# Optimization experiments

Hardware: AMD Instinct MI355X
Metric: run time of the kernel (lower is better)

The kernel has to match this reference:

```python
import jax, jax.numpy as jnp
import numpy as np


def setup_inputs() -> dict:
    key = jax.random.key(0)
    B, S, D, H = 4, 2048, 1024, 16
    hd = D // H
    ks = jax.random.split(key, 11)
    sc = 1.0 / np.sqrt(D)
    return {
        "keys": jax.random.normal(ks[0], (B, S, D), jnp.float32),
        "queries": jax.random.normal(ks[1], (B, S, D), jnp.float32),
        "values": jax.random.normal(ks[2], (B, S, D), jnp.float32),
        "Wq": jax.random.normal(ks[3], (H, D, hd), jnp.float32) * sc,
        "bq": jax.random.normal(ks[4], (H, hd), jnp.float32) * 0.02,
        "Wk": jax.random.normal(ks[5], (H, D, hd), jnp.float32) * sc,
        "bk": jax.random.normal(ks[6], (H, hd), jnp.float32) * 0.02,
        "Wv": jax.random.normal(ks[7], (H, D, hd), jnp.float32) * sc,
        "bv": jax.random.normal(ks[8], (H, hd), jnp.float32) * 0.02,
        "Wo": jax.random.normal(ks[9], (D, D), jnp.float32) * sc,
        "bo": jax.random.normal(ks[10], (D,), jnp.float32) * 0.02,
    }


def reference(keys, queries, values, Wq, bq, Wk, bk, Wv, bv, Wo, bo):
    # Per-head linear projections: [B,S,D] x [H,D,hd] -> [B,H,S,hd]
    q = jnp.einsum("bsd,hde->bhse", queries, Wq) + bq[None, :, None, :]
    k = jnp.einsum("bsd,hde->bhse", keys, Wk) + bk[None, :, None, :]
    v = jnp.einsum("bsd,hde->bhse", values, Wv) + bv[None, :, None, :]

    hd = q.shape[-1]
    S = q.shape[2]
    scores = jnp.einsum("bhse,bhte->bhst", q, k) / jnp.sqrt(jnp.float32(hd))
    causal = jnp.tril(jnp.ones((S, S), dtype=bool))  # tril buffer
    scores = jnp.where(causal[None, None, :, :], scores, -jnp.inf)
    attn = jax.nn.softmax(scores, axis=-1)  # dropout p=0 (eval)

    o = jnp.einsum("bhst,bhte->bhse", attn, v)  # [B,H,S,hd]
    # concat heads -> [B,S,H*hd]
    o = o.transpose(0, 2, 1, 3).reshape(o.shape[0], S, -1)
    return o @ Wo + bo
```

## Files before the change

### kernel.cpp

```cpp
#include <hip/hip_runtime.h>
#include <stdint.h>

typedef unsigned short u16;
typedef __attribute__((ext_vector_type(4))) float f32x4;
typedef __attribute__((ext_vector_type(8))) short bfrag;

static __device__ __forceinline__ u16 f2bf(float f) {
  union { float f; uint32_t u; } v; v.f = f;
  return (u16)((v.u + 0x7fffu + ((v.u >> 16) & 1u)) >> 16);
}
static __device__ __forceinline__ uint32_t cvtpk(float lo, float hi) {
  uint32_t r;
  asm("v_cvt_pk_bf16_f32 %0, %1, %2" : "=v"(r) : "v"(lo), "v"(hi));
  return r;
}
static __device__ __forceinline__ uint32_t pk2bf(float lo, float hi) {
  union { float f; uint32_t u; } a, b; a.f = lo; b.f = hi;
  return __builtin_amdgcn_perm(b.u + 0x8000u, a.u + 0x8000u, 0x07060302u);
}
static __device__ __forceinline__ float fexp2(float x) {
  float r;
  asm("v_exp_f32 %0, %1" : "=v"(r) : "v"(x));
  return r;
}

#define GLOAD16(gp, lp)                                              \
  __builtin_amdgcn_global_load_lds(                                  \
      (const __attribute__((address_space(1))) uint32_t*)(gp),       \
      (__attribute__((address_space(3))) uint32_t*)(lp), 16, 0, 0)

__global__ __launch_bounds__(256) void pack_w_hde(const float* __restrict__ W,
                                                  u16* __restrict__ Wt) {
  __shared__ float tile[64][65];
  const int h = blockIdx.y, k0 = blockIdx.x * 64;
  const int tid = threadIdx.x;
#pragma unroll
  for (int j = 0; j < 4; ++j) {
    int idx = tid + j * 256;
    int rr = idx >> 4, c4 = (idx & 15) * 4;
    const float4 v = *(const float4*)(W + (size_t)h * 65536 + (size_t)(k0 + rr) * 64 + c4);
    tile[rr][c4 + 0] = v.x; tile[rr][c4 + 1] = v.y;
    tile[rr][c4 + 2] = v.z; tile[rr][c4 + 3] = v.w;
  }
  __syncthreads();
#pragma unroll
  for (int j = 0; j < 4; ++j) {
    int idx = tid + j * 256;
    int ee = idx >> 4, c4 = (idx & 15) * 4;
    uint2 u;
    u.x = f2bf(tile[c4 + 0][ee]) | ((uint32_t)f2bf(tile[c4 + 1][ee]) << 16);
    u.y = f2bf(tile[c4 + 2][ee]) | ((uint32_t)f2bf(tile[c4 + 3][ee]) << 16);
    *(uint2*)(Wt + (size_t)(h * 64 + ee) * 1024 + k0 + c4) = u;
  }
}

__global__ __launch_bounds__(256) void transpose_w(const float* __restrict__ W,
                                                   u16* __restrict__ Wt) {
  __shared__ float tile[64][65];
  const int k0 = blockIdx.x * 64, n0 = blockIdx.y * 64;
  const int tid = threadIdx.x;
#pragma unroll
  for (int j = 0; j < 4; ++j) {
    int idx = tid + j * 256;
    int rr = idx >> 4, c4 = (idx & 15) * 4;
    const float4 v = *(const float4*)(W + (size_t)(k0 + rr) * 1024 + n0 + c4);
    tile[rr][c4 + 0] = v.x; tile[rr][c4 + 1] = v.y;
    tile[rr][c4 + 2] = v.z; tile[rr][c4 + 3] = v.w;
  }
  __syncthreads();
#pragma unroll
  for (int j = 0; j < 4; ++j) {
    int idx = tid + j * 256;
    int ee = idx >> 4, c4 = (idx & 15) * 4;
    uint2 u;
    u.x = f2bf(tile[c4 + 0][ee]) | ((uint32_t)f2bf(tile[c4 + 1][ee]) << 16);
    u.y = f2bf(tile[c4 + 2][ee]) | ((uint32_t)f2bf(tile[c4 + 3][ee]) << 16);
    *(uint2*)(Wt + (size_t)(n0 + ee) * 1024 + k0 + c4) = u;
  }
}

__global__ __launch_bounds__(512) void gemm_qkv(
    const float* __restrict__ Aq, const float* __restrict__ Ak,
    const float* __restrict__ Avv, const u16* __restrict__ Bt,
    const float* __restrict__ bq, const float* __restrict__ bk,
    const float* __restrict__ bv,
    u16* __restrict__ Qb, u16* __restrict__ Kb, u16* __restrict__ Vt) {
  __shared__ u16 As[2][128 * 32];
  __shared__ u16 Bs[3][256 * 32];
  const int tid = threadIdx.x;
  const int n = blockIdx.x;
  const int xcd = n & 7, j = n >> 3;
  const int mb = xcd * 8 + (j & 7);
  const int nb2 = j >> 3;
  const int chunk = nb2 >> 2;
  const float* Af = (chunk == 0) ? Aq : (chunk == 1) ? Ak : Avv;
  const int wid = tid >> 6, lane = tid & 63;
  const int wr = wid >> 2, wc = wid & 3;
  const int g = lane >> 4, l15 = lane & 15;
  f32x4 acc[4][4] = {};

  const int bsrc = ((lane & 3) ^ ((lane >> 3) & 3)) * 8;
  const u16* Bg = Bt + (size_t)(nb2 * 256 + 2 * wid * 16 + (lane >> 2)) * 1024 + bsrc;
  const float* Ap = Af + (size_t)(mb * 128 + (tid >> 2)) * 1024 + (tid & 3) * 8;
  const int arow = tid >> 2;
  const int acs = (((tid & 3) ^ ((tid >> 3) & 3))) * 8;
  const int swzr = (l15 >> 1) & 3;
  const int bofs0 = (2 * wid) * 512, bofs1 = (2 * wid + 1) * 512;

  float4 a00 = *(const float4*)(Ap);
  float4 a01 = *(const float4*)(Ap + 4);
  GLOAD16(Bg, &Bs[0][bofs0]);
  GLOAD16(Bg + (size_t)16 * 1024, &Bs[0][bofs1]);
  GLOAD16(Bg + 32, &Bs[1][bofs0]);
  GLOAD16(Bg + (size_t)16 * 1024 + 32, &Bs[1][bofs1]);
  float4 fc0 = *(const float4*)(Ap + 32);
  float4 fc1 = *(const float4*)(Ap + 36);
  {
    uint4 u;
    u.x = pk2bf(a00.x, a00.y); u.y = pk2bf(a00.z, a00.w);
    u.z = pk2bf(a01.x, a01.y); u.w = pk2bf(a01.z, a01.w);
    *(uint4*)&As[0][arow * 32 + acs] = u;
  }
  asm volatile("s_waitcnt vmcnt(4) lgkmcnt(0)" ::: "memory");
  __builtin_amdgcn_s_barrier();

  float4 fn0, fn1;
#pragma unroll 2
  for (int kk = 0; kk < 32; ++kk) {
    const bool more2 = (kk + 2 < 32);
    if (more2) {
      const int kn2 = (kk + 2) * 32;
      fn0 = *(const float4*)(Ap + kn2);
      fn1 = *(const float4*)(Ap + kn2 + 4);
      u16* bd = &Bs[(kk + 2) % 3][0];
      GLOAD16(Bg + kn2, bd + bofs0);
      GLOAD16(Bg + (size_t)16 * 1024 + kn2, bd + bofs1);
    }
    if (kk + 1 < 32) {
      uint4 u;
      u.x = pk2bf(fc0.x, fc0.y); u.y = pk2bf(fc0.z, fc0.w);
      u.z = pk2bf(fc1.x, fc1.y); u.w = pk2bf(fc1.z, fc1.w);
      *(uint4*)&As[(kk + 1) & 1][arow * 32 + acs] = u;
    }
    const u16* AsB = &As[kk & 1][0];
    const u16* BsB = &Bs[kk % 3][0];
    bfrag a[4], b[4];
#pragma unroll
    for (int m = 0; m < 4; ++m)
      a[m] = __builtin_bit_cast(bfrag,
          *(const uint4*)&AsB[(wr * 64 + m * 16 + l15) * 32 + ((g ^ swzr)) * 8]);
#pragma unroll
    for (int nn = 0; nn < 4; ++nn)
      b[nn] = __builtin_bit_cast(bfrag,
          *(const uint4*)&BsB[(wc * 64 + nn * 16 + l15) * 32 + ((g ^ swzr)) * 8]);
    __builtin_amdgcn_s_setprio(1);
#pragma unroll
    for (int m = 0; m < 4; ++m)
#pragma unroll
      for (int nn = 0; nn < 4; ++nn)
        acc[m][nn] = __builtin_amdgcn_mfma_f32_16x16x32_bf16(a[m], b[nn], acc[m][nn], 0, 0, 0);
    __builtin_amdgcn_s_setprio(0);
    if (kk < 31) {
      if (more2)
        asm volatile("s_waitcnt vmcnt(4) lgkmcnt(0)" ::: "memory");
      else
        asm volatile("s_waitcnt vmcnt(0) lgkmcnt(0)" ::: "memory");
      __builtin_amdgcn_s_barrier();
    }
    fc0 = fn0; fc1 = fn1;
  }

  const int row0 = mb * 128 + wr * 64 + g * 4;
  const int ccL = (nb2 & 3) * 256 + wc * 64 + l15;
  const float* bias = (chunk == 0) ? bq : (chunk == 1) ? bk : bv;
  const float qs = (chunk == 0) ? 0.125f * 1.44269504f : 1.0f;
#pragma unroll
  for (int m = 0; m < 4; ++m) {
#pragma unroll
    for (int nn = 0; nn < 4; ++nn) {
      const int row = row0 + m * 16;
      const int cc = ccL + nn * 16;
      const float bcv = bias[cc];
      if (chunk < 2) {
        u16* dst = (chunk == 0) ? Qb : Kb;
#pragma unroll
        for (int r = 0; r < 4; ++r)
          dst[(size_t)(row + r) * 1024 + cc] = f2bf((acc[m][nn][r] + bcv) * qs);
      } else {
        u16 w[4];
#pragma unroll
        for (int r = 0; r < 4; ++r) w[r] = f2bf(acc[m][nn][r] + bcv);
        const size_t dst =
            ((size_t)((row >> 11) * 16 + (cc >> 6)) * 64 + (cc & 63)) * 2048 + (row & 2047);
        *(uint2*)(Vt + dst) = *(const uint2*)w;
      }
    }
  }
}

__global__ __launch_bounds__(256) void gemm_o(const u16* __restrict__ Abf,
                                              const u16* __restrict__ Bt,
                                              const float* __restrict__ bo,
                                              float* __restrict__ Of) {
  __shared__ u16 As[2][128 * 32];
  __shared__ u16 Bs[2][128 * 32];
  const int tid = threadIdx.x;
  const int n = blockIdx.x;
  const int xcd = n & 7, j = n >> 3;
  const int mb = xcd * 8 + (j & 7);
  const int nb = j >> 3;
  const int wid = tid >> 6, lane = tid & 63;
  const int wr = wid >> 1, wc = wid & 1;
  const int g = lane >> 4, l15 = lane & 15;
  f32x4 acc[4][4] = {};

  const int bsrc = ((lane & 3) ^ ((lane >> 3) & 3)) * 8;
  const int swzr = (l15 >> 1) & 3;
  const u16* Bg = Bt + (size_t)(nb * 128 + 2 * wid * 16 + (lane >> 2)) * 1024 + bsrc;
  const u16* Ag = Abf + (size_t)(mb * 128 + 2 * wid * 16 + (lane >> 2)) * 1024 + bsrc;

#pragma unroll
  for (int c = 0; c < 2; ++c) {
    GLOAD16(Ag + (size_t)c * 16 * 1024, &As[0][2 * wid * 512 + c * 512]);
    GLOAD16(Bg + (size_t)c * 16 * 1024, &Bs[0][2 * wid * 512 + c * 512]);
  }
  __syncthreads();
  int cur = 0;
  for (int kk = 0; kk < 32; ++kk) {
    if (kk < 31) {
      const int kn = (kk + 1) * 32;
#pragma unroll
      for (int c = 0; c < 2; ++c) {
        GLOAD16(Ag + (size_t)c * 16 * 1024 + kn, &As[cur ^ 1][2 * wid * 512 + c * 512]);
        GLOAD16(Bg + (size_t)c * 16 * 1024 + kn, &Bs[cur ^ 1][2 * wid * 512 + c * 512]);
      }
    }
    bfrag a[4], b[4];
#pragma unroll
    for (int m = 0; m < 4; ++m)
      a[m] = __builtin_bit_cast(bfrag,
          *(const uint4*)&As[cur][(wr * 64 + m * 16 + l15) * 32 + ((g ^ swzr)) * 8]);
#pragma unroll
    for (int nn = 0; nn < 4; ++nn)
      b[nn] = __builtin_bit_cast(bfrag,
          *(const uint4*)&Bs[cur][(wc * 64 + nn * 16 + l15) * 32 + ((g ^ swzr)) * 8]);
    __builtin_amdgcn_s_setprio(1);
#pragma unroll
    for (int m = 0; m < 4; ++m)
#pragma unroll
      for (int nn = 0; nn < 4; ++nn)
        acc[m][nn] = __builtin_amdgcn_mfma_f32_16x16x32_bf16(a[m], b[nn], acc[m][nn], 0, 0, 0);
    __builtin_amdgcn_s_setprio(0);
    if (kk < 31) { __syncthreads(); cur ^= 1; }
  }

  const int row0 = mb * 128 + wr * 64 + g * 4;
  const int col0 = nb * 128 + wc * 64 + l15;
#pragma unroll
  for (int m = 0; m < 4; ++m)
#pragma unroll
    for (int nn = 0; nn < 4; ++nn) {
      const int row = row0 + m * 16, col = col0 + nn * 16;
      const float bcv = bo[col];
#pragma unroll
      for (int r = 0; r < 4; ++r)
        Of[(size_t)(row + r) * 1024 + col] = acc[m][nn][r] + bcv;
    }
}

__global__ __launch_bounds__(512) void attn_fused(const u16* __restrict__ Qb,
                                                  const u16* __restrict__ Kb,
                                                  const u16* __restrict__ Vtg,
                                                  u16* __restrict__ Ob) {
  __shared__ u16 KV[2][2][4096];
  const int tid = threadIdx.x;
  const int wid = tid >> 6, lane = tid & 63;
  const int g = lane >> 4, l15 = lane & 15;
  const int n = blockIdx.x;
  const int half = n >> 8, idx = n & 255;
  const int xcd = idx & 7;
  const int bh = xcd * 8 + ((idx >> 3) & 7);
  const int grp = idx >> 6;
  const int u = half ? grp : (7 - grp);
  const int t = u * 8 + wid;
  const int b = bh >> 4, h = bh & 15;
  const size_t baserow = (size_t)b * 2048;
  const u16* Qg = Qb + baserow * 1024 + h * 64;
  const u16* Kg = Kb + baserow * 1024 + h * 64;
  const u16* Vg = Vtg + (size_t)bh * 64 * 2048;
  u16* Og = Ob + baserow * 1024 + h * 64;

  const int q0 = t * 32;
  const int qrow = q0 + l15;
  const int mysteps = (q0 >> 6) + 1;
  const int smax = 4 * u + 4;
  const float M2 = 6.0f;

  const int sr = tid >> 3;
  const int scc = (tid & 7) ^ (sr & 7);
  const u16* Kst = Kg + (size_t)sr * 1024 + scc * 8;
  const u16* Vst = Vg + (size_t)sr * 2048 + scc * 8;

  bfrag qa[2][2];
#pragma unroll
  for (int qf = 0; qf < 2; ++qf)
#pragma unroll
    for (int kh = 0; kh < 2; ++kh)
      qa[qf][kh] = __builtin_bit_cast(bfrag,
          *(const uint4*)(Qg + (size_t)(q0 + qf * 16 + l15) * 1024 + kh * 32 + g * 8));

  f32x4 accT[2][4] = {};
  float Ll[2] = {0.f, 0.f};

  const int s0lane = ((g & 1) << 5) | l15;
  const int s1lane = s0lane + 16;
  const bool ghi = (g >= 2);
  const int swz = l15 & 7;

  GLOAD16(Kst, &KV[0][0][wid * 512]);
  GLOAD16(Vst, &KV[0][1][wid * 512]);
  __syncthreads();

  for (int s = 0; s < smax; ++s) {
    const int cb = s & 1;
    if (s + 1 < smax) {
      const size_t kn = (size_t)(s + 1) << 6;
      GLOAD16(Kst + kn * 1024, &KV[cb ^ 1][0][wid * 512]);
      GLOAD16(Vst + kn, &KV[cb ^ 1][1][wid * 512]);
    }
    if (s < mysteps) {
      const int kv0 = s << 6;
      const bool diag = (s == mysteps - 1);
      const u16* KB = &KV[cb][0][0];
      const u16* VB = &KV[cb][1][0];

      bfrag kb[2][4];
#pragma unroll
      for (int tt = 0; tt < 4; ++tt)
#pragma unroll
        for (int kh = 0; kh < 2; ++kh)
          kb[kh][tt] = __builtin_bit_cast(bfrag,
              *(const uint4*)&KB[(tt * 16 + l15) * 64 + (((kh << 2) | g) ^ swz) * 8]);

      f32x4 sc[2][4];
      __builtin_amdgcn_s_setprio(1);
#pragma unroll
      for (int qf = 0; qf < 2; ++qf)
#pragma unroll
        for (int tt = 0; tt < 4; ++tt) {
          f32x4 z = {0.f, 0.f, 0.f, 0.f};
          z = __builtin_amdgcn_mfma_f32_16x16x32_bf16(kb[0][tt], qa[qf][0], z, 0, 0, 0);
          z = __builtin_amdgcn_mfma_f32_16x16x32_bf16(kb[1][tt], qa[qf][1], z, 0, 0, 0);
          sc[qf][tt] = z;
        }
      __builtin_amdgcn_s_setprio(0);

      bfrag vb[2][4];
#pragma unroll
      for (int et = 0; et < 4; ++et)
#pragma unroll
        for (int kcb = 0; kcb < 2; ++kcb)
          vb[kcb][et] = __builtin_bit_cast(bfrag,
              *(const uint4*)&VB[(et * 16 + l15) * 64 + (((kcb << 2) | g) ^ swz) * 8]);

#pragma unroll
      for (int qf = 0; qf < 2; ++qf) {
        if (diag) {
          const int qq = qrow + qf * 16;
#pragma unroll
          for (int tt = 0; tt < 4; ++tt) {
            const int kvb = kv0 + tt * 16 + g * 4;
#pragma unroll
            for (int r = 0; r < 4; ++r)
              sc[qf][tt][r] = (kvb + r <= qq) ? sc[qf][tt][r] : -100.0f;
          }
        }
        uint32_t pk[4][2];
        float ss = 0.f;
#pragma unroll
        for (int tt = 0; tt < 4; ++tt) {
          float p0 = fexp2(sc[qf][tt][0] - M2);
          float p1 = fexp2(sc[qf][tt][1] - M2);
          float p2 = fexp2(sc[qf][tt][2] - M2);
          float p3 = fexp2(sc[qf][tt][3] - M2);
          ss += (p0 + p1) + (p2 + p3);
          pk[tt][0] = cvtpk(p0, p1);
          pk[tt][1] = cvtpk(p2, p3);
        }
        Ll[qf] += ss;
        __builtin_amdgcn_s_setprio(1);
#pragma unroll
        for (int kcb = 0; kcb < 2; ++kcb) {
          const int lo = kcb * 2, hi = kcb * 2 + 1;
          const uint32_t a0 = __shfl(pk[lo][0], s0lane), b0 = __shfl(pk[hi][0], s0lane);
          const uint32_t a1 = __shfl(pk[lo][1], s0lane), b1 = __shfl(pk[hi][1], s0lane);
          const uint32_t a2 = __shfl(pk[lo][0], s1lane), b2 = __shfl(pk[hi][0], s1lane);
          const uint32_t a3 = __shfl(pk[lo][1], s1lane), b3 = __shfl(pk[hi][1], s1lane);
          uint4 uu;
          uu.x = ghi ? b0 : a0; uu.y = ghi ? b1 : a1;
          uu.z = ghi ? b2 : a2; uu.w = ghi ? b3 : a3;
          const bfrag pfrag = __builtin_bit_cast(bfrag, uu);
#pragma unroll
          for (int et = 0; et < 4; ++et)
            accT[qf][et] = __builtin_amdgcn_mfma_f32_16x16x32_bf16(vb[kcb][et], pfrag, accT[qf][et], 0, 0, 0);
        }
        __builtin_amdgcn_s_setprio(0);
      }
    }
    __syncthreads();
  }

#pragma unroll
  for (int qf = 0; qf < 2; ++qf) {
    float Ls = Ll[qf];
    Ls += __shfl_xor(Ls, 16);
    Ls += __shfl_xor(Ls, 32);
    const float inv = 1.f / Ls;
    u16* orow = Og + (size_t)(q0 + qf * 16 + l15) * 1024 + g * 4;
#pragma unroll
    for (int et = 0; et < 4; ++et) {
      uint2 w;
      w.x = cvtpk(accT[qf][et][0] * inv, accT[qf][et][1] * inv);
      w.y = cvtpk(accT[qf][et][2] * inv, accT[qf][et][3] * inv);
      *(uint2*)(orow + et * 16) = w;
    }
  }
}

extern "C" void kernel_launch(void* const* d_in, const int* in_sizes, int n_in,
                              void* d_out, int out_size, void* d_ws, size_t ws_size,
                              hipStream_t stream) {
  const float* keys    = (const float*)d_in[0];
  const float* queries = (const float*)d_in[1];
  const float* values  = (const float*)d_in[2];
  const float* Wq = (const float*)d_in[3];
  const float* bq = (const float*)d_in[4];
  const float* Wk = (const float*)d_in[5];
  const float* bk = (const float*)d_in[6];
  const float* Wv = (const float*)d_in[7];
  const float* bv = (const float*)d_in[8];
  const float* Wo = (const float*)d_in[9];
  const float* bo = (const float*)d_in[10];
  float* out = (float*)d_out;

  char* ws = (char*)d_ws;
  const size_t MB = 1u << 20;
  u16* Wqkvt = (u16*)(ws);
  u16* Wot   = (u16*)(ws + 6 * MB);
  u16* Qb    = (u16*)(ws + 8 * MB);
  u16* Kb    = (u16*)(ws + 24 * MB);
  u16* Vtg   = (u16*)(ws + 40 * MB);
  u16* Ob    = (u16*)(ws + 56 * MB);

  const dim3 pg(16, 16);
  pack_w_hde<<<pg, 256, 0, stream>>>(Wq, Wqkvt);
  pack_w_hde<<<pg, 256, 0, stream>>>(Wk, Wqkvt + (size_t)1024 * 1024);
  pack_w_hde<<<pg, 256, 0, stream>>>(Wv, Wqkvt + (size_t)2048 * 1024);
  transpose_w<<<pg, 256, 0, stream>>>(Wo, Wot);

  gemm_qkv<<<dim3(768), 512, 0, stream>>>(queries, keys, values, Wqkvt,
                                          bq, bk, bv, Qb, Kb, Vtg);

  attn_fused<<<dim3(512), 512, 0, stream>>>(Qb, Kb, Vtg, Ob);

  gemm_o<<<dim3(512), 256, 0, stream>>>(Ob, Wot, bo, out);
}
```

Measured before the change: 184.2 us.

## Pre-convert QKV inputs to bf16 and use 256x256 async-pipelined GEMM

Adds a separate kernel that converts the fp32 query/key/value activations to bf16 in workspace, then runs a new QKV projection GEMM with 256x256 tiles. The GEMM uses direct global-to-LDS loads, double buffering with staged vmcnt waits, and priority hints around the MFMA blocks. This is meant to remove the in-GEMM fp32 conversion and raise MFMA utilization. In exchange it costs an extra full pass over the inputs and needs a larger workspace; when the workspace is too small it falls back to the old kernel.

Result: slower. 202.0 us (+9.7%).

```diff
diff --git a/kernel.cpp b/kernel.cpp
--- a/kernel.cpp
+++ b/kernel.cpp
@@ -76,6 +76,146 @@
     u.x = f2bf(tile[c4 + 0][ee]) | ((uint32_t)f2bf(tile[c4 + 1][ee]) << 16);
     u.y = f2bf(tile[c4 + 2][ee]) | ((uint32_t)f2bf(tile[c4 + 3][ee]) << 16);
     *(uint2*)(Wt + (size_t)(n0 + ee) * 1024 + k0 + c4) = u;
+  }
+}
+
+__global__ __launch_bounds__(256) void conv_bf16(const float* __restrict__ q,
+                                                 const float* __restrict__ k,
+                                                 const float* __restrict__ v,
+                                                 u16* __restrict__ oq,
+                                                 u16* __restrict__ ok,
+                                                 u16* __restrict__ ov) {
+  const float* in = (blockIdx.y == 0) ? q : (blockIdx.y == 1) ? k : v;
+  u16* out = (blockIdx.y == 0) ? oq : (blockIdx.y == 1) ? ok : ov;
+  const size_t i = ((size_t)blockIdx.x * 256 + threadIdx.x) * 8;
+  const float4 f0 = *(const float4*)(in + i);
+  const float4 f1 = *(const float4*)(in + i + 4);
+  uint4 u;
+  u.x = pk2bf(f0.x, f0.y); u.y = pk2bf(f0.z, f0.w);
+  u.z = pk2bf(f1.x, f1.y); u.w = pk2bf(f1.z, f1.w);
+  *(uint4*)(out + i) = u;
+}
+
+__global__ __launch_bounds__(512, 1) void gemm_qkvb8(
+    const u16* __restrict__ cq, const u16* __restrict__ ck,
+    const u16* __restrict__ cv, const u16* __restrict__ Bt,
+    const float* __restrict__ bq, const float* __restrict__ bk,
+    const float* __restrict__ bv,
+    u16* __restrict__ Qb, u16* __restrict__ Kb, u16* __restrict__ Vt) {
+  __shared__ u16 Ab[2][2][8192];
+  __shared__ u16 Bb[2][2][8192];
+  const int tid = threadIdx.x;
+  const int wid = tid >> 6, lane = tid & 63;
+  const int wr = wid >> 2, wc = wid & 3;
+  const int g = lane >> 4, l15 = lane & 15;
+  const int n = blockIdx.x;
+  const int xcd = n & 7, j = n >> 3;
+  const int mb = xcd * 4 + (j & 3);
+  const int nb = j >> 2;
+  const int chunk = nb >> 2, nbl = nb & 3;
+  const u16* Abf = (chunk == 0) ? cq : (chunk == 1) ? ck : cv;
+
+  const int srow = tid >> 3;
+  const int schk = (tid & 7) ^ (srow & 7);
+  const u16* Ag = Abf + (size_t)(mb * 256 + srow) * 1024 + schk * 8;
+  const u16* Bg = Bt + (size_t)(nb * 256 + srow) * 1024 + schk * 8;
+
+  f32x4 acc[8][4] = {};
+
+#define SA(db, hf, i, kt)                                                     \
+  do {                                                                        \
+    GLOAD16(Ag + ((size_t)((hf)*128 + (i)*64)) * 1024 + (kt) * 64,            \
+            &Ab[db][hf][(i)*4096 + tid * 8]);                                 \
+  } while (0)
+#define SB(db, hf, i, kt)                                                     \
+  do {                                                                        \
+    GLOAD16(Bg + ((size_t)((hf)*128 + (i)*64)) * 1024 + (kt) * 64,            \
+            &Bb[db][hf][(i)*4096 + tid * 8]);                                 \
+  } while (0)
+
+  SB(0, 0, 0, 0); SB(0, 0, 1, 0); SB(0, 1, 0, 0); SB(0, 1, 1, 0);
+  SA(0, 0, 0, 0); SA(0, 1, 0, 0); SA(0, 0, 1, 0); SA(0, 1, 1, 0);
+  asm volatile("s_waitcnt vmcnt(0)" ::: "memory");
+  __builtin_amdgcn_s_barrier();
+
+  const int swz = l15 & 7;
+  for (int kt = 0; kt < 16; ++kt) {
+    const int db = kt & 1, dn = db ^ 1;
+    const bool stg = (kt < 15);
+    bfrag bfr[2][4], afr[2][2];
+#pragma unroll
+    for (int mq = 0; mq < 4; ++mq) {
+      if (mq == 0) {
+#pragma unroll
+        for (int nf = 0; nf < 4; ++nf)
+#pragma unroll
+          for (int ks = 0; ks < 2; ++ks)
+            bfr[ks][nf] = __builtin_bit_cast(bfrag,
+                *(const uint4*)&Bb[db][wc >> 1]
+                    [((wc & 1) * 64 + nf * 16 + l15) * 64 + ((ks * 4 + g) ^ swz) * 8]);
+      }
+#pragma unroll
+      for (int m2 = 0; m2 < 2; ++m2)
+#pragma unroll
+        for (int ks = 0; ks < 2; ++ks)
+          afr[ks][m2] = __builtin_bit_cast(bfrag,
+              *(const uint4*)&Ab[db][wr]
+                  [((mq * 2 + m2) * 16 + l15) * 64 + ((ks * 4 + g) ^ swz) * 8]);
+      if (stg) {
+        if (mq == 0)      { SB(dn, 0, 0, kt + 1); SB(dn, 0, 1, kt + 1); }
+        else if (mq == 1) { SB(dn, 1, 0, kt + 1); SB(dn, 1, 1, kt + 1); }
+        else if (mq == 2) { SA(dn, 0, 0, kt + 1); SA(dn, 1, 0, kt + 1); }
+        else              { SA(dn, 0, 1, kt + 1); SA(dn, 1, 1, kt + 1); }
+      }
+      __builtin_amdgcn_s_barrier();
+      __builtin_amdgcn_s_setprio(1);
+#pragma unroll
+      for (int m2 = 0; m2 < 2; ++m2)
+#pragma unroll
+        for (int nf = 0; nf < 4; ++nf) {
+          acc[mq * 2 + m2][nf] = __builtin_amdgcn_mfma_f32_16x16x32_bf16(
+              afr[0][m2], bfr[0][nf], acc[mq * 2 + m2][nf], 0, 0, 0);
+          acc[mq * 2 + m2][nf] = __builtin_amdgcn_mfma_f32_16x16x32_bf16(
+              afr[1][m2], bfr[1][nf], acc[mq * 2 + m2][nf], 0, 0, 0);
+        }
+      __builtin_amdgcn_s_setprio(0);
+      if (mq == 1) {
+        if (stg) asm volatile("s_waitcnt vmcnt(4)" ::: "memory");
+        else     asm volatile("s_waitcnt vmcnt(0)" ::: "memory");
+      } else if (mq == 3 && stg) {
+        asm volatile("s_waitcnt vmcnt(2)" ::: "memory");
+      }
+      __builtin_amdgcn_s_barrier();
+    }
+  }
+#undef SA
+#undef SB
+
+  const int row0 = mb * 256 + wr * 128 + g * 4;
+  const int cc0 = nbl * 256 + wc * 64 + l15;
+  const float* bias = (chunk == 0) ? bq : (chunk == 1) ? bk : bv;
+  const float qs = (chunk == 0) ? 0.125f * 1.44269504f : 1.0f;
+#pragma unroll
+  for (int mf = 0; mf < 8; ++mf) {
+#pragma unroll
+    for (int nf = 0; nf < 4; ++nf) {
+      const int row = row0 + mf * 16;
+      const int cc = cc0 + nf * 16;
+      const float bcv = bias[cc];
+      if (chunk < 2) {
+        u16* dst = (chunk == 0) ? Qb : Kb;
+#pragma unroll
+        for (int r = 0; r < 4; ++r)
+          dst[(size_t)(row + r) * 1024 + cc] = f2bf((acc[mf][nf][r] + bcv) * qs);
+      } else {
+        u16 w[4];
+#pragma unroll
+        for (int r = 0; r < 4; ++r) w[r] = f2bf(acc[mf][nf][r] + bcv);
+        const size_t dst =
+            ((size_t)((row >> 11) * 16 + (cc >> 6)) * 64 + (cc & 63)) * 2048 + (row & 2047);
+        *(uint2*)(Vt + dst) = *(const uint2*)w;
+      }
+    }
   }
 }
 
@@ -451,6 +591,9 @@
   u16* Kb    = (u16*)(ws + 24 * MB);
   u16* Vtg   = (u16*)(ws + 40 * MB);
   u16* Ob    = (u16*)(ws + 56 * MB);
+  u16* cvQ   = (u16*)(ws + 56 * MB);
+  u16* cvK   = (u16*)(ws + 72 * MB);
+  u16* cvV   = (u16*)(ws + 88 * MB);
 
   const dim3 pg(16, 16);
   pack_w_hde<<<pg, 256, 0, stream>>>(Wq, Wqkvt);
@@ -458,8 +601,14 @@
   pack_w_hde<<<pg, 256, 0, stream>>>(Wv, Wqkvt + (size_t)2048 * 1024);
   transpose_w<<<pg, 256, 0, stream>>>(Wo, Wot);
 
-  gemm_qkv<<<dim3(768), 512, 0, stream>>>(queries, keys, values, Wqkvt,
-                                          bq, bk, bv, Qb, Kb, Vtg);
+  if (ws_size >= 104 * MB) {
+    conv_bf16<<<dim3(4096, 3), 256, 0, stream>>>(queries, keys, values, cvQ, cvK, cvV);
+    gemm_qkvb8<<<dim3(384), 512, 0, stream>>>(cvQ, cvK, cvV, Wqkvt,
+                                              bq, bk, bv, Qb, Kb, Vtg);
+  } else {
+    gemm_qkv<<<dim3(768), 512, 0, stream>>>(queries, keys, values, Wqkvt,
+                                            bq, bk, bv, Qb, Kb, Vtg);
+  }
 
   attn_fused<<<dim3(512), 512, 0, stream>>>(Qb, Kb, Vtg, Ob);
 
```
